# Optimization experiments

Measured on AMD Instinct MI355X. Metric: run time of the kernel, lower is better.

The kernel has to match this reference:

```python
import jax, jax.numpy as jnp
import numpy as np

L, H, NH, V, T, B, K = 12, 768, 12, 30522, 512, 4, 21
DH = H // NH
INV_SQRT_DH = 1.0 / float(np.sqrt(DH))
NEG = -1e4  # BERT additive mask value
LN_EPS = 1e-12


def _ln(x, g, b):
    m = x.mean(-1, keepdims=True)
    v = jnp.var(x, axis=-1, keepdims=True)
    return (x - m) * jax.lax.rsqrt(v + LN_EPS) * g + b


def _encoder(input_ids, attention_mask, word_emb, pos_emb, tok_emb, emb_g, emb_b,
             Wqkv, bqkv, Wo, bo, ln1_g, ln1_b, W1, b1, W2, b2, ln2_g, ln2_b):
    Bv, Tv = input_ids.shape
    h = word_emb[input_ids] + pos_emb[None, :Tv] + tok_emb[0]  # token_type_ids = 0
    h = _ln(h, emb_g, emb_b)
    bias = (1.0 - attention_mask[:, None, None, :].astype(h.dtype)) * NEG  # [B,1,1,T]

    def layer(h, xs):
        wqkv, bq, wo, bo_, g1, b1_, w1, bb1, w2, bb2, g2, b2_ = xs
        qkv = h @ wqkv + bq  # [B,T,3H]
        q, k, v = jnp.split(qkv, 3, axis=-1)
        def hd(x):
            return x.reshape(Bv, Tv, NH, DH).transpose(0, 2, 1, 3)
        q, k, v = hd(q), hd(k), hd(v)
        scores = jnp.einsum('bhqd,bhkd->bhqk', q, k) * INV_SQRT_DH + bias
        ctx = jnp.einsum('bhqk,bhkd->bhqd', jax.nn.softmax(scores, axis=-1), v)
        ctx = ctx.transpose(0, 2, 1, 3).reshape(Bv, Tv, H)
        h = _ln(h + ctx @ wo + bo_, g1, b1_)  # post-LN (BERT)
        ff = jax.nn.gelu(h @ w1 + bb1, approximate=False) @ w2 + bb2
        h = _ln(h + ff, g2, b2_)
        return h, None

    h, _ = jax.lax.scan(layer, h, (Wqkv, bqkv, Wo, bo, ln1_g, ln1_b, W1, b1, W2, b2, ln2_g, ln2_b))
    return h


def _crf_nll(emissions, tags, mask, start, end, trans):
    # emissions [B,T,K], tags [B,T] int, mask [B,T] bool; torchcrf reduction='mean'
    Bv, Tv, Kv = emissions.shape
    maskf = mask.astype(emissions.dtype)
    # numerator: score of the gold path
    num = start[tags[:, 0]] + emissions[jnp.arange(Bv), 0, tags[:, 0]]
    em_t = jnp.take_along_axis(emissions, tags[..., None], axis=-1)[..., 0]  # [B,T]
    tr_t = trans[tags[:, :-1], tags[:, 1:]]  # [B,T-1]
    num = num + jnp.sum((tr_t + em_t[:, 1:]) * maskf[:, 1:], axis=1)
    last_idx = mask.sum(axis=1).astype(jnp.int32) - 1
    last_tag = jnp.take_along_axis(tags, last_idx[:, None], axis=1)[:, 0]
    num = num + end[last_tag]
    # denominator: forward algorithm (logsumexp recursion over time)
    alpha0 = start[None, :] + emissions[:, 0]  # [B,K]

    def step(alpha, xs):
        em, m = xs  # em [B,K], m [B] bool
        nxt = jax.scipy.special.logsumexp(alpha[:, :, None] + trans[None] + em[:, None, :], axis=1)
        return jnp.where(m[:, None], nxt, alpha), None

    alpha, _ = jax.lax.scan(step, alpha0, (emissions[:, 1:].transpose(1, 0, 2), mask[:, 1:].T))
    den = jax.scipy.special.logsumexp(alpha + end[None, :], axis=1)
    return -(num - den).mean()


def _viterbi(emissions, mask, start, end, trans):
    # Returns [B,T] int32 best paths; padded tail repeats the last valid tag.
    Bv, Tv, Kv = emissions.shape
    score0 = start[None, :] + emissions[:, 0]
    ident = jnp.broadcast_to(jnp.arange(Kv), (Bv, Kv))

    def step(score, xs):
        em, m = xs
        cand = score[:, :, None] + trans[None]  # [B,K_prev,K_next]
        idx = jnp.where(m[:, None], jnp.argmax(cand, axis=1), ident)
        nxt = jnp.max(cand, axis=1) + em
        return jnp.where(m[:, None], nxt, score), idx

    score, hist = jax.lax.scan(step, score0, (emissions[:, 1:].transpose(1, 0, 2), mask[:, 1:].T))
    last = jnp.argmax(score + end[None, :], axis=1)  # [B]

    def back(nxt_tag, idx):
        prev = jnp.take_along_axis(idx, nxt_tag[:, None], axis=1)[:, 0]
        return prev, nxt_tag

    tag0, rest = jax.lax.scan(back, last, hist, reverse=True)  # rest[i] = tag at t=i+1
    return jnp.concatenate([tag0[None], rest], axis=0).T.astype(jnp.int32)


def setup_inputs():
    key = jax.random.key(0)
    ks = jax.random.split(key, 16)
    s = 0.02

    def n(k, shape):
        return (s * jax.random.normal(k, shape)).astype(jnp.float32)

    def u(k, shape):
        return jax.random.uniform(k, shape, minval=-0.1, maxval=0.1).astype(jnp.float32)

    p = {}
    p['input_ids'] = jax.random.randint(ks[0], (B, T), 0, V)
    lengths = jax.random.randint(ks[1], (B,), T // 2, T + 1)
    p['attention_mask'] = (jnp.arange(T)[None, :] < lengths[:, None]).astype(jnp.int32)
    p['valid_mask'] = p['attention_mask']
    p['labels'] = jax.random.randint(ks[2], (B, T), 0, K)
    p['word_emb'] = n(ks[3], (V, H))
    p['pos_emb'] = n(ks[4], (T, H))
    p['tok_emb'] = n(ks[5], (2, H))
    p['emb_g'] = jnp.ones((H,), jnp.float32)
    p['emb_b'] = jnp.zeros((H,), jnp.float32)
    p['Wqkv'] = n(ks[6], (L, H, 3 * H))
    p['bqkv'] = jnp.zeros((L, 3 * H), jnp.float32)
    p['Wo'] = n(ks[7], (L, H, H))
    p['bo'] = jnp.zeros((L, H), jnp.float32)
    p['ln1_g'] = jnp.ones((L, H), jnp.float32)
    p['ln1_b'] = jnp.zeros((L, H), jnp.float32)
    p['W1'] = n(ks[8], (L, H, 4 * H))
    p['b1'] = jnp.zeros((L, 4 * H), jnp.float32)
    p['W2'] = n(ks[9], (L, 4 * H, H))
    p['b2'] = jnp.zeros((L, H), jnp.float32)
    p['ln2_g'] = jnp.ones((L, H), jnp.float32)
    p['ln2_b'] = jnp.zeros((L, H), jnp.float32)
    p['Wc'] = n(ks[10], (H, K))
    p['bc'] = jnp.zeros((K,), jnp.float32)
    p['crf_start'] = u(ks[11], (K,))
    p['crf_end'] = u(ks[12], (K,))
    p['crf_trans'] = u(ks[13], (K, K))
    return p


def reference(input_ids, attention_mask, valid_mask, labels,
              word_emb, pos_emb, tok_emb, emb_g, emb_b,
              Wqkv, bqkv, Wo, bo, ln1_g, ln1_b, W1, b1, W2, b2, ln2_g, ln2_b,
              Wc, bc, crf_start, crf_end, crf_trans):
    h = _encoder(input_ids, attention_mask, word_emb, pos_emb, tok_emb, emb_g, emb_b,
                 Wqkv, bqkv, Wo, bo, ln1_g, ln1_b, W1, b1, W2, b2, ln2_g, ln2_b)
    emissions = h @ Wc + bc  # dropout is identity in eval/reference mode
    mask = attention_mask.astype(bool)
    nll = _crf_nll(emissions, labels, mask, crf_start, crf_end, crf_trans)
    decoded = _viterbi(emissions, mask, crf_start, crf_end, crf_trans)
    return nll, decoded
```

## Files before the change

kernel.cpp:

```cpp
#include <hip/hip_runtime.h>
#include <math.h>

constexpr int NLAYER = 12;
constexpr int H = 768;
constexpr int NH = 12;
constexpr int DH = 64;
constexpr int T = 512;
constexpr int B = 4;
constexpr int K = 21;
constexpr int BT = B * T;
constexpr float NEGB = -10000.0f;
constexpr float LNEPS = 1e-12f;
constexpr float INV_SQRT_DH = 0.125f;

typedef __attribute__((ext_vector_type(8))) short bf16x8;
typedef __attribute__((ext_vector_type(4))) float f32x4;
typedef __attribute__((ext_vector_type(4))) unsigned short u16x4;

#define WAIT_VMCNT(n) asm volatile("s_waitcnt vmcnt(" #n ")")

__device__ __forceinline__ float wave_sum_f(float v) {
#pragma unroll
  for (int off = 32; off > 0; off >>= 1) v += __shfl_xor(v, off);
  return v;
}
__device__ __forceinline__ int wave_sum_i(int v) {
#pragma unroll
  for (int off = 32; off > 0; off >>= 1) v += __shfl_xor(v, off);
  return v;
}
__device__ __forceinline__ float readlane_f(float v, int i) {
  return __uint_as_float(__builtin_amdgcn_readlane(__float_as_uint(v), i));
}
__device__ __forceinline__ unsigned short f32_bf16_rn(float x) {
  unsigned int u = __float_as_uint(x);
  u += 0x7fffu + ((u >> 16) & 1u);
  return (unsigned short)(u >> 16);
}
__device__ __forceinline__ void split_bf16(float x, unsigned short& h, unsigned short& l) {
  h = f32_bf16_rn(x);
  float hf = __uint_as_float((unsigned int)h << 16);
  l = f32_bf16_rn(x - hf);
}
__device__ __forceinline__ void block_reduce_sum2(float& s, float& q) {
  __shared__ float red[8];
  s = wave_sum_f(s);
  q = wave_sum_f(q);
  int lane = threadIdx.x & 63, wid = threadIdx.x >> 6;
  if (lane == 0) { red[wid] = s; red[4 + wid] = q; }
  __syncthreads();
  s = red[0] + red[1] + red[2] + red[3];
  q = red[4] + red[5] + red[6] + red[7];
}

__global__ __launch_bounds__(256) void embed_ln_kernel(
    const int* __restrict__ ids, const float* __restrict__ wemb,
    const float* __restrict__ pemb, const float* __restrict__ temb,
    const float* __restrict__ g, const float* __restrict__ bta,
    float* __restrict__ h, unsigned short* __restrict__ hh,
    unsigned short* __restrict__ hl) {
  int row = blockIdx.x;
  int t = row % T;
  int id = ids[row];
  const float* wp = wemb + (size_t)id * H;
  const float* pp = pemb + (size_t)t * H;
  float x[3];
  float s = 0.f, q = 0.f;
#pragma unroll
  for (int i = 0; i < 3; i++) {
    int c = threadIdx.x + i * 256;
    x[i] = wp[c] + pp[c] + temb[c];
    s += x[i];
    q += x[i] * x[i];
  }
  block_reduce_sum2(s, q);
  float mean = s * (1.0f / H);
  float var = q * (1.0f / H) - mean * mean;
  float inv = rsqrtf(var + LNEPS);
#pragma unroll
  for (int i = 0; i < 3; i++) {
    int c = threadIdx.x + i * 256;
    float y = (x[i] - mean) * inv * g[c] + bta[c];
    h[(size_t)row * H + c] = y;
    unsigned short yh, yl;
    split_bf16(y, yh, yl);
    hh[(size_t)row * H + c] = yh;
    hl[(size_t)row * H + c] = yl;
  }
}

__global__ __launch_bounds__(256) void add_ln_kernel(
    float* __restrict__ h, const float* __restrict__ add,
    const float* __restrict__ g, const float* __restrict__ bta,
    unsigned short* __restrict__ hh, unsigned short* __restrict__ hl) {
  int row = blockIdx.x;
  size_t base = (size_t)row * H;
  float x[3];
  float s = 0.f, q = 0.f;
#pragma unroll
  for (int i = 0; i < 3; i++) {
    int c = threadIdx.x + i * 256;
    x[i] = h[base + c] + add[base + c];
    s += x[i];
    q += x[i] * x[i];
  }
  block_reduce_sum2(s, q);
  float mean = s * (1.0f / H);
  float var = q * (1.0f / H) - mean * mean;
  float inv = rsqrtf(var + LNEPS);
#pragma unroll
  for (int i = 0; i < 3; i++) {
    int c = threadIdx.x + i * 256;
    float y = (x[i] - mean) * inv * g[c] + bta[c];
    h[base + c] = y;
    unsigned short yh, yl;
    split_bf16(y, yh, yl);
    hh[base + c] = yh;
    hl[base + c] = yl;
  }
}

__global__ __launch_bounds__(256) void wconv_kernel(
    const float* __restrict__ w0, const float* __restrict__ w1,
    const float* __restrict__ w2, const float* __restrict__ w3,
    unsigned short* __restrict__ Wth, unsigned short* __restrict__ Wtl) {
  __shared__ float tile[32][33];
  int bid = blockIdx.x;
  const float* src;
  int Kd, N, tk, tn;
  size_t off;
  if (bid < 1728) {
    src = w0; Kd = 768; N = 2304; tk = bid / 72; tn = bid % 72; off = 0;
  } else if (bid < 2304) {
    int t2 = bid - 1728; src = w1; Kd = 768; N = 768; tk = t2 / 24; tn = t2 % 24;
    off = 1769472;
  } else if (bid < 4608) {
    int t2 = bid - 2304; src = w2; Kd = 768; N = 3072; tk = t2 / 96; tn = t2 % 96;
    off = 2359296;
  } else {
    int t2 = bid - 4608; src = w3; Kd = 3072; N = 768; tk = t2 / 24; tn = t2 % 24;
    off = 4718592;
  }
  int tid = threadIdx.x;
  int k0 = tk * 32, n0 = tn * 32;
  int r = tid >> 3, c = (tid & 7) * 4;
  float4 v = *(const float4*)(src + (size_t)(k0 + r) * N + n0 + c);
  tile[r][c + 0] = v.x; tile[r][c + 1] = v.y; tile[r][c + 2] = v.z; tile[r][c + 3] = v.w;
  __syncthreads();
  u16x4 hv, lv;
#pragma unroll
  for (int q2 = 0; q2 < 4; q2++) {
    unsigned short sh, sl;
    split_bf16(tile[c + q2][r], sh, sl);
    hv[q2] = sh; lv[q2] = sl;
  }
  size_t dst = off + (size_t)(n0 + r) * Kd + k0 + c;
  *(u16x4*)(Wth + dst) = hv;
  *(u16x4*)(Wtl + dst) = lv;
}

template <int OUTMODE>
__global__ __launch_bounds__(256) void gemm_bf3_kernel(
    const unsigned short* __restrict__ Ah, const unsigned short* __restrict__ Al,
    const unsigned short* __restrict__ Wth, const unsigned short* __restrict__ Wtl,
    const float* __restrict__ bias, float* __restrict__ C,
    unsigned short* __restrict__ Ch, unsigned short* __restrict__ Cl,
    unsigned short* __restrict__ Kh, unsigned short* __restrict__ Kl,
    unsigned short* __restrict__ Vth, unsigned short* __restrict__ Vtl,
    int N, int Kd, int ncols) {
  constexpr int AW = 64 * 32;
  constexpr int WW = 128 * 32;
  constexpr int DBS = 2 * AW + 2 * WW;
  __shared__ short lds_s[2 * DBS];
  int tid = threadIdx.x;
  int lane = tid & 63, wid = tid >> 6;
  int wr = wid >> 1, wc = wid & 1;
  int tiles = gridDim.x;
  int q8 = tiles >> 3;
  int wg = (blockIdx.x & 7) * q8 + (blockIdx.x >> 3);
  int bm = (wg / ncols) * 64, bn = (wg % ncols) * 128;

  f32x4 acc[2][4] = {};
  int lrow = lane >> 2;
  int lslot_sw = (lane & 3) ^ ((lrow >> 1) & 3);

  const unsigned short* sbase;
  int rowbase, ldsoff, nchunks;
  if (wid == 0)      { sbase = Ah;  rowbase = bm; ldsoff = 0;            nchunks = 4; }
  else if (wid == 1) { sbase = Al;  rowbase = bm; ldsoff = AW;           nchunks = 4; }
  else if (wid == 2) { sbase = Wth; rowbase = bn; ldsoff = 2 * AW;       nchunks = 8; }
  else               { sbase = Wtl; rowbase = bn; ldsoff = 2 * AW + WW;  nchunks = 8; }

  const unsigned short* srcbase = sbase + (size_t)(rowbase + lrow) * Kd + lslot_sw * 8;

  auto STAGE = [&](int db, int k0) {
#pragma unroll
    for (int c = 0; c < 8; c++) {
      if (c < nchunks) {
        const unsigned short* src = srcbase + (size_t)(c * 16) * Kd + k0;
        char* dst = ((char*)lds_s) + (db * DBS + ldsoff) * 2 + c * 1024 + lane * 16;
        __builtin_amdgcn_global_load_lds(
            (const __attribute__((address_space(1))) void*)src,
            (__attribute__((address_space(3))) void*)dst, 16, 0, 0);
      }
    }
  };

  const int NT = Kd / 32;
  STAGE(0, 0);
  for (int kt = 0; kt < NT; kt++) {
    int cur = kt & 1;
    bool more = (kt + 1 < NT);
    if (more) STAGE(cur ^ 1, (kt + 1) * 32);
    if (more) {
      if (wid < 2) { WAIT_VMCNT(4); } else { WAIT_VMCNT(8); }
    } else {
      WAIT_VMCNT(0);
    }
    __builtin_amdgcn_s_barrier();
    __builtin_amdgcn_sched_barrier(0);

    int lr = lane & 15, lg = lane >> 4;
    int slot = (lg ^ ((lr >> 1) & 3)) * 8;
    int cb = cur * DBS;
    bf16x8 af_h[2], af_l[2], wf_h[4], wf_l[4];
#pragma unroll
    for (int i = 0; i < 2; i++) {
      int e = (wr * 32 + i * 16 + lr) * 32 + slot;
      af_h[i] = *(const bf16x8*)&lds_s[cb + e];
      af_l[i] = *(const bf16x8*)&lds_s[cb + AW + e];
    }
#pragma unroll
    for (int j = 0; j < 4; j++) {
      int e = (wc * 64 + j * 16 + lr) * 32 + slot;
      wf_h[j] = *(const bf16x8*)&lds_s[cb + 2 * AW + e];
      wf_l[j] = *(const bf16x8*)&lds_s[cb + 2 * AW + WW + e];
    }
#pragma unroll
    for (int i = 0; i < 2; i++)
#pragma unroll
      for (int j = 0; j < 4; j++) {
        acc[i][j] = __builtin_amdgcn_mfma_f32_16x16x32_bf16(af_h[i], wf_h[j], acc[i][j], 0, 0, 0);
        acc[i][j] = __builtin_amdgcn_mfma_f32_16x16x32_bf16(af_l[i], wf_h[j], acc[i][j], 0, 0, 0);
        acc[i][j] = __builtin_amdgcn_mfma_f32_16x16x32_bf16(af_h[i], wf_l[j], acc[i][j], 0, 0, 0);
      }
    asm volatile("s_waitcnt lgkmcnt(0)");
    __builtin_amdgcn_sched_barrier(0);
    __builtin_amdgcn_s_barrier();
    __builtin_amdgcn_sched_barrier(0);
  }

  int lr = lane & 15, lg = lane >> 4;
#pragma unroll
  for (int i = 0; i < 2; i++) {
#pragma unroll
    for (int j = 0; j < 4; j++) {
      int row = bm + wr * 32 + i * 16 + lg * 4;
      int col = bn + wc * 64 + j * 16 + lr;
      float bv = bias[col];
      if (OUTMODE == 2) {
        int sec = col / 768;
        int within = col % 768;
        int hidx = within >> 6, d = within & 63;
        int b = row >> 9, t = row & 511;
        int bh = b * NH + hidx;
        if (sec == 2) {
          u16x4 hv, lv;
#pragma unroll
          for (int r = 0; r < 4; r++) {
            unsigned short sh, sl;
            split_bf16(acc[i][j][r] + bv, sh, sl);
            hv[r] = sh; lv[r] = sl;
          }
          size_t idx = ((size_t)bh * 64 + d) * T + t;
          *(u16x4*)(Vth + idx) = hv;
          *(u16x4*)(Vtl + idx) = lv;
        } else {
          unsigned short* dh = (sec == 0) ? Ch : Kh;
          unsigned short* dl = (sec == 0) ? Cl : Kl;
#pragma unroll
          for (int r = 0; r < 4; r++) {
            unsigned short sh, sl;
            split_bf16(acc[i][j][r] + bv, sh, sl);
            size_t idx = ((size_t)bh * T + t + r) * 64 + d;
            dh[idx] = sh;
            dl[idx] = sl;
          }
        }
      } else {
#pragma unroll
        for (int r = 0; r < 4; r++) {
          float v = acc[i][j][r] + bv;
          if (OUTMODE == 1) {
            v = 0.5f * v * (1.0f + erff(v * 0.70710678118654752f));
            unsigned short sh, sl;
            split_bf16(v, sh, sl);
            Ch[(size_t)(row + r) * N + col] = sh;
            Cl[(size_t)(row + r) * N + col] = sl;
          } else {
            C[(size_t)(row + r) * N + col] = v;
          }
        }
      }
    }
  }
}

__global__ __launch_bounds__(256) void attn_kernel(
    const unsigned short* __restrict__ qh, const unsigned short* __restrict__ ql,
    const unsigned short* __restrict__ kh, const unsigned short* __restrict__ kl,
    const unsigned short* __restrict__ vth, const unsigned short* __restrict__ vtl,
    const int* __restrict__ mask,
    unsigned short* __restrict__ cth, unsigned short* __restrict__ ctl) {
  int bh = blockIdx.y;
  int b = bh / NH, hidx = bh % NH;
  int i0 = blockIdx.x * 64;
  int tid = threadIdx.x, lane = tid & 63, w = tid >> 6;
  int lr = lane & 15, lg = lane >> 4;
  __shared__ float bias_s[T];
  __shared__ short p_h[4][16 * 64];
  __shared__ short p_l[4][16 * 64];
  for (int i = tid; i < T; i += 256)
    bias_s[i] = (1.0f - (float)mask[b * T + i]) * NEGB;
  __syncthreads();

  const unsigned short* qb_h = qh + ((size_t)bh * T + i0 + w * 16 + lr) * 64 + lg * 8;
  const unsigned short* qb_l = ql + ((size_t)bh * T + i0 + w * 16 + lr) * 64 + lg * 8;
  bf16x8 qf_h0 = *(const bf16x8*)qb_h;
  bf16x8 qf_h1 = *(const bf16x8*)(qb_h + 32);
  bf16x8 qf_l0 = *(const bf16x8*)qb_l;
  bf16x8 qf_l1 = *(const bf16x8*)(qb_l + 32);

  float m_run[4], l_run[4];
#pragma unroll
  for (int r = 0; r < 4; r++) { m_run[r] = -3.0e38f; l_run[r] = 0.f; }
  f32x4 acc_o[4] = {};

  for (int kt = 0; kt < T / 64; kt++) {
    f32x4 s[4] = {};
#pragma unroll
    for (int jf = 0; jf < 4; jf++) {
      size_t kb = ((size_t)bh * T + kt * 64 + jf * 16 + lr) * 64 + lg * 8;
      bf16x8 kf_h0 = *(const bf16x8*)(kh + kb);
      bf16x8 kf_h1 = *(const bf16x8*)(kh + kb + 32);
      bf16x8 kf_l0 = *(const bf16x8*)(kl + kb);
      bf16x8 kf_l1 = *(const bf16x8*)(kl + kb + 32);
      s[jf] = __builtin_amdgcn_mfma_f32_16x16x32_bf16(qf_h0, kf_h0, s[jf], 0, 0, 0);
      s[jf] = __builtin_amdgcn_mfma_f32_16x16x32_bf16(qf_h1, kf_h1, s[jf], 0, 0, 0);
      s[jf] = __builtin_amdgcn_mfma_f32_16x16x32_bf16(qf_l0, kf_h0, s[jf], 0, 0, 0);
      s[jf] = __builtin_amdgcn_mfma_f32_16x16x32_bf16(qf_l1, kf_h1, s[jf], 0, 0, 0);
      s[jf] = __builtin_amdgcn_mfma_f32_16x16x32_bf16(qf_h0, kf_l0, s[jf], 0, 0, 0);
      s[jf] = __builtin_amdgcn_mfma_f32_16x16x32_bf16(qf_h1, kf_l1, s[jf], 0, 0, 0);
    }
    float mt[4] = {-3.0e38f, -3.0e38f, -3.0e38f, -3.0e38f};
#pragma unroll
    for (int jf = 0; jf < 4; jf++) {
      float bcol = bias_s[kt * 64 + jf * 16 + lr];
#pragma unroll
      for (int r = 0; r < 4; r++) {
        float v = s[jf][r] * INV_SQRT_DH + bcol;
        s[jf][r] = v;
        mt[r] = fmaxf(mt[r], v);
      }
    }
#pragma unroll
    for (int r = 0; r < 4; r++) {
      mt[r] = fmaxf(mt[r], __shfl_xor(mt[r], 1));
      mt[r] = fmaxf(mt[r], __shfl_xor(mt[r], 2));
      mt[r] = fmaxf(mt[r], __shfl_xor(mt[r], 4));
      mt[r] = fmaxf(mt[r], __shfl_xor(mt[r], 8));
    }
#pragma unroll
    for (int r = 0; r < 4; r++) {
      float mn = fmaxf(m_run[r], mt[r]);
      float sc = __expf(m_run[r] - mn);
      m_run[r] = mn;
      l_run[r] *= sc;
#pragma unroll
      for (int jf = 0; jf < 4; jf++) acc_o[jf][r] *= sc;
    }
    float ps[4] = {0.f, 0.f, 0.f, 0.f};
#pragma unroll
    for (int jf = 0; jf < 4; jf++) {
#pragma unroll
      for (int r = 0; r < 4; r++) {
        float p = __expf(s[jf][r] - m_run[r]);
        ps[r] += p;
        unsigned short sh, sl;
        split_bf16(p, sh, sl);
        int q = lg * 4 + r;
        int col = jf * 16 + lr;
        int addr = q * 64 + (((col >> 3) ^ (q & 7)) << 3) + (col & 7);
        p_h[w][addr] = sh;
        p_l[w][addr] = sl;
      }
    }
#pragma unroll
    for (int r = 0; r < 4; r++) {
      ps[r] += __shfl_xor(ps[r], 1);
      ps[r] += __shfl_xor(ps[r], 2);
      ps[r] += __shfl_xor(ps[r], 4);
      ps[r] += __shfl_xor(ps[r], 8);
      l_run[r] += ps[r];
    }
#pragma unroll
    for (int c = 0; c < 2; c++) {
      int aaddr = lr * 64 + (((4 * c + lg) ^ (lr & 7)) << 3);
      bf16x8 pa_h = *(const bf16x8*)&p_h[w][aaddr];
      bf16x8 pa_l = *(const bf16x8*)&p_l[w][aaddr];
#pragma unroll
      for (int jf = 0; jf < 4; jf++) {
        size_t vb = ((size_t)bh * 64 + jf * 16 + lr) * T + kt * 64 + c * 32 + lg * 8;
        bf16x8 vf_h = *(const bf16x8*)(vth + vb);
        bf16x8 vf_l = *(const bf16x8*)(vtl + vb);
        acc_o[jf] = __builtin_amdgcn_mfma_f32_16x16x32_bf16(pa_h, vf_h, acc_o[jf], 0, 0, 0);
        acc_o[jf] = __builtin_amdgcn_mfma_f32_16x16x32_bf16(pa_l, vf_h, acc_o[jf], 0, 0, 0);
        acc_o[jf] = __builtin_amdgcn_mfma_f32_16x16x32_bf16(pa_h, vf_l, acc_o[jf], 0, 0, 0);
      }
    }
  }
  float inv[4];
#pragma unroll
  for (int r = 0; r < 4; r++) inv[r] = 1.0f / l_run[r];
#pragma unroll
  for (int jf = 0; jf < 4; jf++) {
#pragma unroll
    for (int r = 0; r < 4; r++) {
      float v = acc_o[jf][r] * inv[r];
      unsigned short sh, sl;
      split_bf16(v, sh, sl);
      size_t idx = ((size_t)(b * T) + i0 + w * 16 + lg * 4 + r) * H + hidx * 64 + jf * 16 + lr;
      cth[idx] = sh;
      ctl[idx] = sl;
    }
  }
}

__global__ __launch_bounds__(256) void wct_kernel(
    const float* __restrict__ Wc, float* __restrict__ WcT) {
  int id = blockIdx.x * 256 + threadIdx.x;
  int k = id / H, d = id % H;
  WcT[id] = Wc[d * K + k];
}

__global__ __launch_bounds__(256) void classifier_kernel(
    const float* __restrict__ h, const float* __restrict__ WcT,
    const float* __restrict__ bc, float* __restrict__ em) {
  int id = blockIdx.x * 256 + threadIdx.x;
  if (id >= BT * K) return;
  int row = id / K, k = id % K;
  const float4* h4 = (const float4*)(h + (size_t)row * H);
  const float4* w4 = (const float4*)(WcT + (size_t)k * H);
  float acc = bc[k];
  for (int d = 0; d < H / 4; d++) {
    float4 a = h4[d], b = w4[d];
    acc = fmaf(a.x, b.x, acc);
    acc = fmaf(a.y, b.y, acc);
    acc = fmaf(a.z, b.z, acc);
    acc = fmaf(a.w, b.w, acc);
  }
  em[id] = acc;
}

#define MRG(vo, io, va, ia, vb, ib) \
  float vo = ((vb) > (va)) ? (vb) : (va); \
  int io = ((vb) > (va)) ? (ib) : (ia);

__global__ __launch_bounds__(64) void crf_fused_kernel(
    const float* __restrict__ em, const int* __restrict__ labels,
    const int* __restrict__ mask, const float* __restrict__ start,
    const float* __restrict__ endv, const float* __restrict__ trans,
    float* __restrict__ parts, float* __restrict__ outdec) {
  __shared__ float em_s[T * K];
  __shared__ int mask_s[T];
  __shared__ unsigned char hist_s[(T - 1) * K];
  __shared__ float sc_s[32];
  int b = blockIdx.x & 3;
  int role = blockIdx.x >> 2;
  int j = threadIdx.x;
  const float* eb = em + (size_t)b * T * K;
  for (int i = j; i < T * K / 4; i += 64)
    ((float4*)em_s)[i] = ((const float4*)eb)[i];
  for (int i = j; i < T; i += 64) mask_s[i] = mask[b * T + i];
  __syncthreads();
  bool act = (j < K);
  float tr[K];
#pragma unroll
  for (int i = 0; i < K; i++) tr[i] = act ? trans[i * K + j] : 0.f;

  int cntloc = 0;
  for (int t = j; t < T; t += 64) cntloc += mask_s[t];
  int cnt = wave_sum_i(cntloc);

  if (role == 0) {
    const int* tb = labels + b * T;
    float numloc = 0.f;
    for (int t = j; t < T; t += 64) {
      if (t >= 1 && mask_s[t]) {
        int tp = tb[t - 1], tc = tb[t];
        numloc += trans[tp * K + tc] + em_s[t * K + tc];
      }
    }
    float num = wave_sum_f(numloc);
    float etr[K];
#pragma unroll
    for (int i = 0; i < K; i++) etr[i] = __expf(tr[i]);
    float alpha = act ? (start[j] + em_s[j]) : 0.f;
    float emv = act ? em_s[K + j] : 0.f;
    for (int t = 1; t < cnt; t++) {
      float emv_n = (act && (t + 1) < cnt) ? em_s[(t + 1) * K + j] : 0.f;
      float m0 = readlane_f(alpha, 0);
      float ee = __expf(alpha - m0);
      float e0 = readlane_f(ee, 0),  e1 = readlane_f(ee, 1),  e2 = readlane_f(ee, 2);
      float e3 = readlane_f(ee, 3),  e4 = readlane_f(ee, 4),  e5 = readlane_f(ee, 5);
      float e6 = readlane_f(ee, 6),  e7 = readlane_f(ee, 7),  e8 = readlane_f(ee, 8);
      float e9 = readlane_f(ee, 9),  e10 = readlane_f(ee, 10), e11 = readlane_f(ee, 11);
      float e12 = readlane_f(ee, 12), e13 = readlane_f(ee, 13), e14 = readlane_f(ee, 14);
      float e15 = readlane_f(ee, 15), e16 = readlane_f(ee, 16), e17 = readlane_f(ee, 17);
      float e18 = readlane_f(ee, 18), e19 = readlane_f(ee, 19), e20 = readlane_f(ee, 20);
      float a0 = fmaf(e16, etr[16], fmaf(e12, etr[12], fmaf(e8, etr[8],  fmaf(e4, etr[4], e0 * etr[0]))));
      float a1 = fmaf(e17, etr[17], fmaf(e13, etr[13], fmaf(e9, etr[9],  fmaf(e5, etr[5], e1 * etr[1]))));
      float a2 = fmaf(e18, etr[18], fmaf(e14, etr[14], fmaf(e10, etr[10], fmaf(e6, etr[6], e2 * etr[2]))));
      float a3 = fmaf(e19, etr[19], fmaf(e15, etr[15], fmaf(e11, etr[11], fmaf(e7, etr[7], e3 * etr[3]))));
      float ssum = fmaf(e20, etr[20], (a0 + a1) + (a2 + a3));
      float nxt = __logf(ssum) + m0 + emv;
      if (act) alpha = nxt;
      emv = emv_n;
    }
    float aj = act ? (alpha + endv[j]) : -3.0e38f;
    float mm = aj;
#pragma unroll
    for (int off = 32; off > 0; off >>= 1) mm = fmaxf(mm, __shfl_xor(mm, off));
    float e2v = act ? __expf(aj - mm) : 0.f;
    float s2 = wave_sum_f(e2v);
    float den = __logf(s2) + mm;
    if (j == 0) {
      int tag0 = tb[0];
      float numtot = num + start[tag0] + em_s[tag0] + endv[tb[cnt - 1]];
      parts[b] = numtot - den;
    }
  } else {
    float score = act ? (start[j] + em_s[j]) : 0.f;
    float emv = act ? em_s[K + j] : 0.f;
    for (int t = 1; t < cnt; t++) {
      float emv_n = (act && (t + 1) < cnt) ? em_s[(t + 1) * K + j] : 0.f;
      float c0 = readlane_f(score, 0) + tr[0],   c1 = readlane_f(score, 1) + tr[1];
      float c2 = readlane_f(score, 2) + tr[2],   c3 = readlane_f(score, 3) + tr[3];
      float c4 = readlane_f(score, 4) + tr[4],   c5 = readlane_f(score, 5) + tr[5];
      float c6 = readlane_f(score, 6) + tr[6],   c7 = readlane_f(score, 7) + tr[7];
      float c8 = readlane_f(score, 8) + tr[8],   c9 = readlane_f(score, 9) + tr[9];
      float c10 = readlane_f(score, 10) + tr[10], c11 = readlane_f(score, 11) + tr[11];
      float c12 = readlane_f(score, 12) + tr[12], c13 = readlane_f(score, 13) + tr[13];
      float c14 = readlane_f(score, 14) + tr[14], c15 = readlane_f(score, 15) + tr[15];
      float c16 = readlane_f(score, 16) + tr[16], c17 = readlane_f(score, 17) + tr[17];
      float c18 = readlane_f(score, 18) + tr[18], c19 = readlane_f(score, 19) + tr[19];
      float c20 = readlane_f(score, 20) + tr[20];
      MRG(m0v, m0i, c0, 0, c1, 1)
      MRG(m1v, m1i, c2, 2, c3, 3)
      MRG(m2v, m2i, c4, 4, c5, 5)
      MRG(m3v, m3i, c6, 6, c7, 7)
      MRG(m4v, m4i, c8, 8, c9, 9)
      MRG(m5v, m5i, c10, 10, c11, 11)
      MRG(m6v, m6i, c12, 12, c13, 13)
      MRG(m7v, m7i, c14, 14, c15, 15)
      MRG(m8v, m8i, c16, 16, c17, 17)
      MRG(m9v, m9i, c18, 18, c19, 19)
      MRG(p0v, p0i, m0v, m0i, m1v, m1i)
      MRG(p1v, p1i, m2v, m2i, m3v, m3i)
      MRG(p2v, p2i, m4v, m4i, m5v, m5i)
      MRG(p3v, p3i, m6v, m6i, m7v, m7i)
      MRG(p4v, p4i, m8v, m8i, m9v, m9i)
      MRG(r0v, r0i, p0v, p0i, p1v, p1i)
      MRG(r1v, r1i, p2v, p2i, p3v, p3i)
      MRG(r2v, r2i, p4v, p4i, c20, 20)
      MRG(s0v, s0i, r0v, r0i, r1v, r1i)
      MRG(fv, fi, s0v, s0i, r2v, r2i)
      if (act) {
        hist_s[(t - 1) * K + j] = (unsigned char)fi;
        score = fv + emv;
      }
      emv = emv_n;
    }
    if (act) sc_s[j] = score + endv[j];
    __syncthreads();
    if (j == 0) {
      float best = -3.0e38f;
      int last = 0;
#pragma unroll
      for (int i = 0; i < K; i++)
        if (sc_s[i] > best) { best = sc_s[i]; last = i; }
      for (int t = cnt - 1; t < T; t++) outdec[b * T + t] = (float)last;
      int cur = last;
      for (int t = cnt - 1; t >= 1; t--) {
        cur = hist_s[(t - 1) * K + cur];
        outdec[b * T + (t - 1)] = (float)cur;
      }
    }
  }
}

__global__ void nll_final_kernel(const float* __restrict__ parts,
                                 float* __restrict__ out) {
  out[0] = -0.25f * (parts[0] + parts[1] + parts[2] + parts[3]);
}

extern "C" void kernel_launch(void* const* d_in, const int* in_sizes, int n_in,
                              void* d_out, int out_size, void* d_ws, size_t ws_size,
                              hipStream_t stream) {
  (void)in_sizes; (void)n_in; (void)out_size; (void)ws_size;
  const int* ids    = (const int*)d_in[0];
  const int* amask  = (const int*)d_in[1];
  const int* labels = (const int*)d_in[3];
  const float* wemb = (const float*)d_in[4];
  const float* pemb = (const float*)d_in[5];
  const float* temb = (const float*)d_in[6];
  const float* eg   = (const float*)d_in[7];
  const float* ebta = (const float*)d_in[8];
  const float* Wqkv = (const float*)d_in[9];
  const float* bqkv = (const float*)d_in[10];
  const float* Wo   = (const float*)d_in[11];
  const float* bo   = (const float*)d_in[12];
  const float* ln1g = (const float*)d_in[13];
  const float* ln1b = (const float*)d_in[14];
  const float* W1   = (const float*)d_in[15];
  const float* b1   = (const float*)d_in[16];
  const float* W2   = (const float*)d_in[17];
  const float* b2   = (const float*)d_in[18];
  const float* ln2g = (const float*)d_in[19];
  const float* ln2b = (const float*)d_in[20];
  const float* Wc   = (const float*)d_in[21];
  const float* bc   = (const float*)d_in[22];
  const float* cst  = (const float*)d_in[23];
  const float* cen  = (const float*)d_in[24];
  const float* ctr  = (const float*)d_in[25];
  float* out = (float*)d_out;

  float* ws = (float*)d_ws;
  float* fp = ws;
  float* h = fp;                 fp += 1572864;
  unsigned short* hh  = (unsigned short*)fp; fp += 786432;
  unsigned short* hl  = (unsigned short*)fp; fp += 786432;
  unsigned short* qhp = (unsigned short*)fp; fp += 786432;
  unsigned short* qlp = (unsigned short*)fp; fp += 786432;
  unsigned short* khp = (unsigned short*)fp; fp += 786432;
  unsigned short* klp = (unsigned short*)fp; fp += 786432;
  unsigned short* vtp = (unsigned short*)fp; fp += 786432;
  unsigned short* vlp = (unsigned short*)fp; fp += 786432;
  unsigned short* cth = (unsigned short*)fp; fp += 786432;
  unsigned short* ctl = (unsigned short*)fp; fp += 786432;
  float* tmp = fp;               fp += 1572864;
  unsigned short* gh  = (unsigned short*)fp; fp += 3145728;
  unsigned short* gl  = (unsigned short*)fp; fp += 3145728;
  unsigned short* Wth = (unsigned short*)fp; fp += 3538944;
  unsigned short* Wtl = (unsigned short*)fp; fp += 3538944;
  float* em = fp;                fp += 43008;
  float* parts = fp;             fp += 8;
  float* WcT = fp;               fp += 16128;

  embed_ln_kernel<<<BT, 256, 0, stream>>>(ids, wemb, pemb, temb, eg, ebta, h, hh, hl);
  wct_kernel<<<63, 256, 0, stream>>>(Wc, WcT);

  for (int l = 0; l < NLAYER; l++) {
    const float* bqkv_l = bqkv + (size_t)l * 3 * H;
    const float* bo_l   = bo + (size_t)l * H;
    const float* b1_l   = b1 + (size_t)l * 4 * H;
    const float* b2_l   = b2 + (size_t)l * H;

    wconv_kernel<<<6912, 256, 0, stream>>>(
        Wqkv + (size_t)l * H * 3 * H, Wo + (size_t)l * H * H,
        W1 + (size_t)l * H * 4 * H, W2 + (size_t)l * 4 * H * H, Wth, Wtl);

    gemm_bf3_kernel<2><<<576, 256, 0, stream>>>(
        hh, hl, Wth, Wtl, bqkv_l, nullptr, qhp, qlp, khp, klp, vtp, vlp,
        3 * H, H, 18);
    attn_kernel<<<dim3(T / 64, B * NH), 256, 0, stream>>>(
        qhp, qlp, khp, klp, vtp, vlp, amask, cth, ctl);
    gemm_bf3_kernel<0><<<192, 256, 0, stream>>>(
        cth, ctl, Wth + 1769472, Wtl + 1769472, bo_l, tmp,
        nullptr, nullptr, nullptr, nullptr, nullptr, nullptr, H, H, 6);
    add_ln_kernel<<<BT, 256, 0, stream>>>(h, tmp, ln1g + (size_t)l * H, ln1b + (size_t)l * H, hh, hl);
    gemm_bf3_kernel<1><<<768, 256, 0, stream>>>(
        hh, hl, Wth + 2359296, Wtl + 2359296, b1_l, nullptr, gh, gl,
        nullptr, nullptr, nullptr, nullptr, 4 * H, H, 24);
    gemm_bf3_kernel<0><<<192, 256, 0, stream>>>(
        gh, gl, Wth + 4718592, Wtl + 4718592, b2_l, tmp,
        nullptr, nullptr, nullptr, nullptr, nullptr, nullptr, H, 4 * H, 6);
    add_ln_kernel<<<BT, 256, 0, stream>>>(h, tmp, ln2g + (size_t)l * H, ln2b + (size_t)l * H, hh, hl);
  }

  classifier_kernel<<<(BT * K + 255) / 256, 256, 0, stream>>>(h, WcT, bc, em);
  crf_fused_kernel<<<8, 64, 0, stream>>>(em, labels, amask, cst, cen, ctr, parts, out + 1);
  nll_final_kernel<<<1, 1, 0, stream>>>(parts, out);
}
```

Before: 3.221 ms.

## Batch all-layer weight conversion into one launch and merge CRF blocks

When the workspace is large enough, all twelve layers' weights are converted to transposed bf16 hi/lo planes in a single up-front launch, replacing twelve per-layer conversion launches. The GEMMs then index per-layer offsets into those planes. The CRF kernel becomes one 512-thread block with eight waves, each reading emissions straight from global memory rather than staging them into shared memory. This trades extra workspace memory, and possibly higher global-load latency in the serial CRF recursion, for fewer launches and a better-filled GPU during conversion.

```diff
diff --git a/kernel.cpp b/kernel.cpp
--- a/kernel.cpp
+++ b/kernel.cpp
@@ -16,6 +16,8 @@
 typedef __attribute__((ext_vector_type(8))) short bf16x8;
 typedef __attribute__((ext_vector_type(4))) float f32x4;
 typedef __attribute__((ext_vector_type(4))) unsigned short u16x4;
+
+constexpr size_t WL_SHORTS = 7077888;
 
 #define WAIT_VMCNT(n) asm volatile("s_waitcnt vmcnt(" #n ")")
 
@@ -121,26 +123,34 @@
 }
 
 __global__ __launch_bounds__(256) void wconv_kernel(
-    const float* __restrict__ w0, const float* __restrict__ w1,
-    const float* __restrict__ w2, const float* __restrict__ w3,
-    unsigned short* __restrict__ Wth, unsigned short* __restrict__ Wtl) {
+    const float* __restrict__ Wqkv, const float* __restrict__ Wo,
+    const float* __restrict__ W1, const float* __restrict__ W2,
+    unsigned short* __restrict__ Wth, unsigned short* __restrict__ Wtl,
+    int lbase) {
   __shared__ float tile[32][33];
-  int bid = blockIdx.x;
+  int li = blockIdx.x / 6912;
+  int bid = blockIdx.x % 6912;
+  int l = lbase + li;
   const float* src;
   int Kd, N, tk, tn;
   size_t off;
   if (bid < 1728) {
-    src = w0; Kd = 768; N = 2304; tk = bid / 72; tn = bid % 72; off = 0;
+    src = Wqkv + (size_t)l * 768 * 2304;
+    Kd = 768; N = 2304; tk = bid / 72; tn = bid % 72; off = 0;
   } else if (bid < 2304) {
-    int t2 = bid - 1728; src = w1; Kd = 768; N = 768; tk = t2 / 24; tn = t2 % 24;
-    off = 1769472;
+    int t2 = bid - 1728;
+    src = Wo + (size_t)l * 768 * 768;
+    Kd = 768; N = 768; tk = t2 / 24; tn = t2 % 24; off = 1769472;
   } else if (bid < 4608) {
-    int t2 = bid - 2304; src = w2; Kd = 768; N = 3072; tk = t2 / 96; tn = t2 % 96;
-    off = 2359296;
+    int t2 = bid - 2304;
+    src = W1 + (size_t)l * 768 * 3072;
+    Kd = 768; N = 3072; tk = t2 / 96; tn = t2 % 96; off = 2359296;
   } else {
-    int t2 = bid - 4608; src = w3; Kd = 3072; N = 768; tk = t2 / 24; tn = t2 % 24;
-    off = 4718592;
-  }
+    int t2 = bid - 4608;
+    src = W2 + (size_t)l * 3072 * 768;
+    Kd = 3072; N = 768; tk = t2 / 24; tn = t2 % 24; off = 4718592;
+  }
+  off += (size_t)li * WL_SHORTS;
   int tid = threadIdx.x;
   int k0 = tk * 32, n0 = tn * 32;
   int r = tid >> 3, c = (tid & 7) * 4;
@@ -466,49 +476,44 @@
   float vo = ((vb) > (va)) ? (vb) : (va); \
   int io = ((vb) > (va)) ? (ib) : (ia);
 
-__global__ __launch_bounds__(64) void crf_fused_kernel(
+__global__ __launch_bounds__(512) void crf_fused_kernel(
     const float* __restrict__ em, const int* __restrict__ labels,
     const int* __restrict__ mask, const float* __restrict__ start,
     const float* __restrict__ endv, const float* __restrict__ trans,
     float* __restrict__ parts, float* __restrict__ outdec) {
-  __shared__ float em_s[T * K];
-  __shared__ int mask_s[T];
-  __shared__ unsigned char hist_s[(T - 1) * K];
-  __shared__ float sc_s[32];
-  int b = blockIdx.x & 3;
-  int role = blockIdx.x >> 2;
-  int j = threadIdx.x;
+  __shared__ unsigned char hist_s[4][(T - 1) * K];
+  __shared__ float sc_s[4][32];
+  int tid = threadIdx.x;
+  int w = tid >> 6, j = tid & 63;
+  int b = w & 3, role = w >> 2;
   const float* eb = em + (size_t)b * T * K;
-  for (int i = j; i < T * K / 4; i += 64)
-    ((float4*)em_s)[i] = ((const float4*)eb)[i];
-  for (int i = j; i < T; i += 64) mask_s[i] = mask[b * T + i];
-  __syncthreads();
+  const int* mb = mask + b * T;
   bool act = (j < K);
   float tr[K];
 #pragma unroll
   for (int i = 0; i < K; i++) tr[i] = act ? trans[i * K + j] : 0.f;
 
   int cntloc = 0;
-  for (int t = j; t < T; t += 64) cntloc += mask_s[t];
+  for (int t = j; t < T; t += 64) cntloc += mb[t];
   int cnt = wave_sum_i(cntloc);
 
   if (role == 0) {
     const int* tb = labels + b * T;
     float numloc = 0.f;
     for (int t = j; t < T; t += 64) {
-      if (t >= 1 && mask_s[t]) {
+      if (t >= 1 && mb[t]) {
         int tp = tb[t - 1], tc = tb[t];
-        numloc += trans[tp * K + tc] + em_s[t * K + tc];
+        numloc += trans[tp * K + tc] + eb[(size_t)t * K + tc];
       }
     }
     float num = wave_sum_f(numloc);
     float etr[K];
 #pragma unroll
     for (int i = 0; i < K; i++) etr[i] = __expf(tr[i]);
-    float alpha = act ? (start[j] + em_s[j]) : 0.f;
-    float emv = act ? em_s[K + j] : 0.f;
+    float alpha = act ? (start[j] + eb[j]) : 0.f;
+    float emv = act ? eb[K + j] : 0.f;
     for (int t = 1; t < cnt; t++) {
-      float emv_n = (act && (t + 1) < cnt) ? em_s[(t + 1) * K + j] : 0.f;
+      float emv_n = (act && (t + 1) < cnt) ? eb[(size_t)(t + 1) * K + j] : 0.f;
       float m0 = readlane_f(alpha, 0);
       float ee = __expf(alpha - m0);
       float e0 = readlane_f(ee, 0),  e1 = readlane_f(ee, 1),  e2 = readlane_f(ee, 2);
@@ -536,14 +541,14 @@
     float den = __logf(s2) + mm;
     if (j == 0) {
       int tag0 = tb[0];
-      float numtot = num + start[tag0] + em_s[tag0] + endv[tb[cnt - 1]];
+      float numtot = num + start[tag0] + eb[tag0] + endv[tb[cnt - 1]];
       parts[b] = numtot - den;
     }
   } else {
-    float score = act ? (start[j] + em_s[j]) : 0.f;
-    float emv = act ? em_s[K + j] : 0.f;
+    float score = act ? (start[j] + eb[j]) : 0.f;
+    float emv = act ? eb[K + j] : 0.f;
     for (int t = 1; t < cnt; t++) {
-      float emv_n = (act && (t + 1) < cnt) ? em_s[(t + 1) * K + j] : 0.f;
+      float emv_n = (act && (t + 1) < cnt) ? eb[(size_t)(t + 1) * K + j] : 0.f;
       float c0 = readlane_f(score, 0) + tr[0],   c1 = readlane_f(score, 1) + tr[1];
       float c2 = readlane_f(score, 2) + tr[2],   c3 = readlane_f(score, 3) + tr[3];
       float c4 = readlane_f(score, 4) + tr[4],   c5 = readlane_f(score, 5) + tr[5];
@@ -576,23 +581,22 @@
       MRG(s0v, s0i, r0v, r0i, r1v, r1i)
       MRG(fv, fi, s0v, s0i, r2v, r2i)
       if (act) {
-        hist_s[(t - 1) * K + j] = (unsigned char)fi;
+        hist_s[b][(t - 1) * K + j] = (unsigned char)fi;
         score = fv + emv;
       }
       emv = emv_n;
     }
-    if (act) sc_s[j] = score + endv[j];
-    __syncthreads();
+    if (act) sc_s[b][j] = score + endv[j];
     if (j == 0) {
       float best = -3.0e38f;
       int last = 0;
 #pragma unroll
       for (int i = 0; i < K; i++)
-        if (sc_s[i] > best) { best = sc_s[i]; last = i; }
+        if (sc_s[b][i] > best) { best = sc_s[b][i]; last = i; }
       for (int t = cnt - 1; t < T; t++) outdec[b * T + t] = (float)last;
       int cur = last;
       for (int t = cnt - 1; t >= 1; t--) {
-        cur = hist_s[(t - 1) * K + cur];
+        cur = hist_s[b][(t - 1) * K + cur];
         outdec[b * T + (t - 1)] = (float)cur;
       }
     }
@@ -607,7 +611,7 @@
 extern "C" void kernel_launch(void* const* d_in, const int* in_sizes, int n_in,
                               void* d_out, int out_size, void* d_ws, size_t ws_size,
                               hipStream_t stream) {
-  (void)in_sizes; (void)n_in; (void)out_size; (void)ws_size;
+  (void)in_sizes; (void)n_in; (void)out_size;
   const int* ids    = (const int*)d_in[0];
   const int* amask  = (const int*)d_in[1];
   const int* labels = (const int*)d_in[3];
@@ -651,14 +655,19 @@
   float* tmp = fp;               fp += 1572864;
   unsigned short* gh  = (unsigned short*)fp; fp += 3145728;
   unsigned short* gl  = (unsigned short*)fp; fp += 3145728;
-  unsigned short* Wth = (unsigned short*)fp; fp += 3538944;
-  unsigned short* Wtl = (unsigned short*)fp; fp += 3538944;
   float* em = fp;                fp += 43008;
   float* parts = fp;             fp += 8;
   float* WcT = fp;               fp += 16128;
+  unsigned short* Wth = (unsigned short*)fp;
+  size_t base_bytes = (size_t)((char*)Wth - (char*)ws);
+  bool big = ws_size >= base_bytes + (size_t)2 * NLAYER * WL_SHORTS * 2 + 1024;
+  size_t plane = big ? (size_t)NLAYER * WL_SHORTS : WL_SHORTS;
+  unsigned short* Wtl = Wth + plane;
 
   embed_ln_kernel<<<BT, 256, 0, stream>>>(ids, wemb, pemb, temb, eg, ebta, h, hh, hl);
   wct_kernel<<<63, 256, 0, stream>>>(Wc, WcT);
+  if (big)
+    wconv_kernel<<<NLAYER * 6912, 256, 0, stream>>>(Wqkv, Wo, W1, W2, Wth, Wtl, 0);
 
   for (int l = 0; l < NLAYER; l++) {
     const float* bqkv_l = bqkv + (size_t)l * 3 * H;
@@ -666,29 +675,29 @@
     const float* b1_l   = b1 + (size_t)l * 4 * H;
     const float* b2_l   = b2 + (size_t)l * H;
 
-    wconv_kernel<<<6912, 256, 0, stream>>>(
-        Wqkv + (size_t)l * H * 3 * H, Wo + (size_t)l * H * H,
-        W1 + (size_t)l * H * 4 * H, W2 + (size_t)l * 4 * H * H, Wth, Wtl);
+    if (!big)
+      wconv_kernel<<<6912, 256, 0, stream>>>(Wqkv, Wo, W1, W2, Wth, Wtl, l);
+    size_t woff = big ? (size_t)l * WL_SHORTS : 0;
 
     gemm_bf3_kernel<2><<<576, 256, 0, stream>>>(
-        hh, hl, Wth, Wtl, bqkv_l, nullptr, qhp, qlp, khp, klp, vtp, vlp,
-        3 * H, H, 18);
+        hh, hl, Wth + woff, Wtl + woff, bqkv_l, nullptr, qhp, qlp, khp, klp,
+        vtp, vlp, 3 * H, H, 18);
     attn_kernel<<<dim3(T / 64, B * NH), 256, 0, stream>>>(
         qhp, qlp, khp, klp, vtp, vlp, amask, cth, ctl);
     gemm_bf3_kernel<0><<<192, 256, 0, stream>>>(
-        cth, ctl, Wth + 1769472, Wtl + 1769472, bo_l, tmp,
+        cth, ctl, Wth + woff + 1769472, Wtl + woff + 1769472, bo_l, tmp,
         nullptr, nullptr, nullptr, nullptr, nullptr, nullptr, H, H, 6);
     add_ln_kernel<<<BT, 256, 0, stream>>>(h, tmp, ln1g + (size_t)l * H, ln1b + (size_t)l * H, hh, hl);
     gemm_bf3_kernel<1><<<768, 256, 0, stream>>>(
-        hh, hl, Wth + 2359296, Wtl + 2359296, b1_l, nullptr, gh, gl,
+        hh, hl, Wth + woff + 2359296, Wtl + woff + 2359296, b1_l, nullptr, gh, gl,
         nullptr, nullptr, nullptr, nullptr, 4 * H, H, 24);
     gemm_bf3_kernel<0><<<192, 256, 0, stream>>>(
-        gh, gl, Wth + 4718592, Wtl + 4718592, b2_l, tmp,
+        gh, gl, Wth + woff + 4718592, Wtl + woff + 4718592, b2_l, tmp,
         nullptr, nullptr, nullptr, nullptr, nullptr, nullptr, H, 4 * H, 6);
     add_ln_kernel<<<BT, 256, 0, stream>>>(h, tmp, ln2g + (size_t)l * H, ln2b + (size_t)l * H, hh, hl);
   }
 
   classifier_kernel<<<(BT * K + 255) / 256, 256, 0, stream>>>(h, WcT, bc, em);
-  crf_fused_kernel<<<8, 64, 0, stream>>>(em, labels, amask, cst, cen, ctr, parts, out + 1);
+  crf_fused_kernel<<<1, 512, 0, stream>>>(em, labels, amask, cst, cen, ctr, parts, out + 1);
   nll_final_kernel<<<1, 1, 0, stream>>>(parts, out);
 }
```

Measured after the change: 4.087 ms. 26.9% more time.
